# Kernel optimization log

Measured on AMD Instinct MI355X. Metric: run time of the kernel, lower is better.

Reference implementation:

```python
import jax, jax.numpy as jnp
import numpy as np
import math

B, S, D, H = 2, 2048, 1024, 16
DH = D // H  # head_dim = 64
NEG = -10000.0


def setup_inputs() -> dict:
    key = jax.random.key(0)
    ks = jax.random.split(key, 6)
    scale = 1.0 / math.sqrt(D)
    inp = {
        "query": jax.random.normal(ks[0], (B, S, D), dtype=jnp.float32),
        "key": jax.random.normal(ks[1], (B, S, D), dtype=jnp.float32),
        "value": jax.random.normal(ks[2], (B, S, D), dtype=jnp.float32),
        "Wq": jax.random.normal(ks[3], (D, D), dtype=jnp.float32) * scale,
        "Wk": jax.random.normal(ks[4], (D, D), dtype=jnp.float32) * scale,
        "Wv": jax.random.normal(ks[5], (D, D), dtype=jnp.float32) * scale,
        "pad_mask": jnp.ones((B, 1, 1, S), dtype=jnp.int32),
        "attn_mask": jnp.tril(jnp.ones((S, S), dtype=jnp.int32))[None, None],  # causal [1,1,S,S]
    }
    return inp


def reference(query, key, value, Wq, Wk, Wv, pad_mask, attn_mask):
    b, s, d = query.shape
    # torch Linear(bias=False): y = x @ W.T ; then split into heads [B,H,S,DH]
    def proj(x, W):
        return (x @ W.T).reshape(b, -1, H, DH).transpose(0, 2, 1, 3)

    Q = proj(query, Wq)
    K = proj(key, Wk)
    V = proj(value, Wv)

    scores = jnp.einsum("bhqd,bhkd->bhqk", Q, K) / math.sqrt(DH)
    scores = jnp.where(attn_mask == 0, NEG, scores)
    scores = jnp.where(pad_mask == 0, NEG, scores)
    attn = jax.nn.softmax(scores, axis=-1)  # dropout p=0.0 -> identity
    ctx = jnp.einsum("bhqk,bhkd->bhqd", attn, V)
    return ctx.transpose(0, 2, 1, 3).reshape(b, -1, d)
```

## Files before the change

kernel.cpp:

```cpp
#include <hip/hip_runtime.h>


typedef unsigned short u16;
typedef unsigned int u32;
typedef u16 u16x4 __attribute__((ext_vector_type(4)));
typedef u16 u16x8 __attribute__((ext_vector_type(8)));
typedef u32 u32x2 __attribute__((ext_vector_type(2)));
typedef u32 u32x4 __attribute__((ext_vector_type(4)));
typedef __bf16 bf16x8 __attribute__((ext_vector_type(8)));
typedef float f32x4 __attribute__((ext_vector_type(4)));

static __device__ __forceinline__ u16 f2bf(float f) {
  unsigned u = __builtin_bit_cast(unsigned, f);
  return (u16)((u + 0x7FFFu + ((u >> 16) & 1u)) >> 16);
}

static __device__ __forceinline__ u32 cvt_pk_bf16(float lo, float hi) {
  u32 r;
  asm("v_cvt_pk_bf16_f32 %0, %1, %2" : "=v"(r) : "v"(lo), "v"(hi));
  return r;
}

static __device__ __forceinline__ u16x8 cvt8(float4 f0, float4 f1) {
  u32x4 v;
  v[0] = cvt_pk_bf16(f0.x, f0.y);
  v[1] = cvt_pk_bf16(f0.z, f0.w);
  v[2] = cvt_pk_bf16(f1.x, f1.y);
  v[3] = cvt_pk_bf16(f1.z, f1.w);
  return __builtin_bit_cast(u16x8, v);
}

static __device__ __forceinline__ f32x4 mfma16(u16x8 a, u16x8 b, f32x4 c) {
  return __builtin_amdgcn_mfma_f32_16x16x32_bf16(
      __builtin_bit_cast(bf16x8, a), __builtin_bit_cast(bf16x8, b), c, 0, 0, 0);
}

static __device__ __forceinline__ float bperm_f(int lane, float v) {
  return __builtin_bit_cast(
      float, __builtin_amdgcn_ds_bpermute(lane * 4, __builtin_bit_cast(int, v)));
}

#define GLOAD16(GSRC, LDST)                                                  \
  __builtin_amdgcn_global_load_lds(                                         \
      (const __attribute__((address_space(1))) unsigned int*)(GSRC),        \
      (__attribute__((address_space(3))) unsigned int*)(LDST), 16, 0, 0)

#define FENCE() asm volatile("" ::: "memory")
#define BARX()                        \
  do {                                \
    __builtin_amdgcn_s_barrier();     \
    FENCE();                          \
  } while (0)

__global__ __launch_bounds__(256) void wconv_kernel(
    const float* __restrict__ Wq, const float* __restrict__ Wk,
    const float* __restrict__ Wv, u16* __restrict__ dst) {
  const float* src = (blockIdx.y == 0) ? Wq : (blockIdx.y == 1) ? Wk : Wv;
  u16* d = dst + (size_t)blockIdx.y * (1024 * 1024);
  const int i = (blockIdx.x * 256 + threadIdx.x) * 8;
  const float4 f0 = *(const float4*)(src + i);
  const float4 f1 = *(const float4*)(src + i + 4);
  *(u16x8*)(d + i) = cvt8(f0, f1);
}

__global__ __launch_bounds__(256) void proj_kernel(
    const float* __restrict__ Xq, const float* __restrict__ Xk, const float* __restrict__ Xv,
    const u16* __restrict__ Wbf,
    u16* __restrict__ Qb, u16* __restrict__ Kb, u16* __restrict__ Vt) {
  const int d0 = blockIdx.x;
  const int tid = (d0 & 7) * 96 + (d0 >> 3);
  const int nI = tid % 24, mI = tid / 24;
  const int mode = nI >> 3;
  const int m0 = mI * 128;
  const int n0 = (nI & 7) * 128;

  const float* __restrict__ X = (mode == 0) ? Xq : (mode == 1) ? Xk : Xv;
  const u16* __restrict__ W = Wbf + (size_t)mode * (1024 * 1024);

  __shared__ __align__(16) u16 As[3][128 * 32];
  __shared__ __align__(16) u16 Bs[3][128 * 32];

  const int t = threadIdx.x;
  const int lane = t & 63;
  const int w = t >> 6;
  const int wm = w >> 1, wn = w & 1;
  const int lr = lane & 15, lg = lane >> 4;

  const int srow0 = w * 32 + (lane >> 2);
  const int srow1 = srow0 + 16;
  const int skoff = ((lane & 3) ^ ((lane >> 3) & 3)) * 8;
  const int ldsb0 = w * 2048 + lane * 16;
  const int ldsb1 = ldsb0 + 1024;

  const float* Xr0 = X + (size_t)(m0 + srow0) * 1024 + skoff;
  const float* Xr1 = X + (size_t)(m0 + srow1) * 1024 + skoff;
  const u16* Wr0 = W + (size_t)(n0 + srow0) * 1024 + skoff;
  const u16* Wr1 = W + (size_t)(n0 + srow1) * 1024 + skoff;

  float4 a0_, a1_, a2_, a3_;

#define ISSUE_A(T)                                   \
  do {                                               \
    const float* _p0 = Xr0 + (T) * 32;               \
    const float* _p1 = Xr1 + (T) * 32;               \
    a0_ = ((const float4*)_p0)[0];                   \
    a1_ = ((const float4*)_p0)[1];                   \
    a2_ = ((const float4*)_p1)[0];                   \
    a3_ = ((const float4*)_p1)[1];                   \
  } while (0)
#define WRITE_A(BUF)                                                 \
  do {                                                               \
    *(u16x8*)((char*)As[BUF] + ldsb0) = cvt8(a0_, a1_);              \
    *(u16x8*)((char*)As[BUF] + ldsb1) = cvt8(a2_, a3_);              \
  } while (0)
#define ISSUE_B(T, BUF)                                              \
  do {                                                               \
    GLOAD16(Wr0 + (T) * 32, (char*)Bs[BUF] + w * 2048);              \
    GLOAD16(Wr1 + (T) * 32, (char*)Bs[BUF] + w * 2048 + 1024);       \
  } while (0)

  f32x4 acc[4][4] = {};
  const int rx = (lr >> 1) & 3;

#define CMP(BUF)                                                              \
  do {                                                                       \
    u16x8 af[4], bfr[4];                                                     \
    _Pragma("unroll") for (int mi = 0; mi < 4; ++mi) {                        \
      const int row = wm * 64 + mi * 16 + lr;                                \
      af[mi] = *(const u16x8*)((char*)As[BUF] + row * 64 + ((lg ^ rx) << 4)); \
    }                                                                         \
    _Pragma("unroll") for (int ni = 0; ni < 4; ++ni) {                        \
      const int row = wn * 64 + ni * 16 + lr;                                \
      bfr[ni] = *(const u16x8*)((char*)Bs[BUF] + row * 64 + ((lg ^ rx) << 4));\
    }                                                                         \
    _Pragma("unroll") for (int mi = 0; mi < 4; ++mi)                          \
        _Pragma("unroll") for (int ni = 0; ni < 4; ++ni)                      \
            acc[mi][ni] = mfma16(af[mi], bfr[ni], acc[mi][ni]);               \
  } while (0)

  ISSUE_A(0); WRITE_A(0);
  ISSUE_A(1); WRITE_A(1);
  ISSUE_A(2);
  ISSUE_B(0, 0);
  ISSUE_B(1, 1);
  asm volatile("s_waitcnt vmcnt(2) lgkmcnt(0)" ::: "memory");
  BARX();

  CMP(0);
  BARX();
  WRITE_A(2);
  ISSUE_A(3);
  ISSUE_B(2, 2);

  for (int tt = 1; tt <= 29; ++tt) {
    asm volatile("s_waitcnt vmcnt(6) lgkmcnt(0)" ::: "memory");
    BARX();
    CMP(tt % 3);
    BARX();
    WRITE_A((tt + 2) % 3);
    if (tt < 29) ISSUE_A(tt + 3);
    ISSUE_B(tt + 2, (tt + 2) % 3);
  }

  asm volatile("s_waitcnt vmcnt(2) lgkmcnt(0)" ::: "memory");
  BARX();
  CMP(30 % 3);
  asm volatile("s_waitcnt vmcnt(0) lgkmcnt(0)" ::: "memory");
  BARX();
  CMP(31 % 3);
#undef ISSUE_A
#undef WRITE_A
#undef ISSUE_B
#undef CMP

#pragma unroll
  for (int mi = 0; mi < 4; ++mi) {
    const int sbase = m0 + wm * 64 + mi * 16 + lg * 4;
    const int b_ = sbase >> 11;
    const int s_ = sbase & 2047;
#pragma unroll
    for (int ni = 0; ni < 4; ++ni) {
      const int n = n0 + wn * 64 + ni * 16 + lr;
      const int h_ = n >> 6, dh = n & 63;
      if (mode == 2) {
        u16x4 pk;
        pk[0] = f2bf(acc[mi][ni][0]);
        pk[1] = f2bf(acc[mi][ni][1]);
        pk[2] = f2bf(acc[mi][ni][2]);
        pk[3] = f2bf(acc[mi][ni][3]);
        *(u16x4*)(Vt + ((size_t)((b_ * 16 + h_) * 64 + dh)) * 2048 + s_) = pk;
      } else {
        const float sc = (mode == 0) ? 0.18033688f : 1.0f;
        u16* dst = (mode == 0 ? Qb : Kb) + (size_t)(b_ * 16 + h_) * (2048 * 64) + dh;
#pragma unroll
        for (int r = 0; r < 4; ++r)
          dst[(size_t)(s_ + r) * 64] = f2bf(acc[mi][ni][r] * sc);
      }
    }
  }
}

__global__ __launch_bounds__(256, 2) void attn_kernel(
    const u16* __restrict__ Qb, const u16* __restrict__ Kb, const u16* __restrict__ Vt,
    const int* __restrict__ pad, float* __restrict__ out) {
  const int id = blockIdx.x;
  const int g = id >> 8, r_ = id & 255;
  const int bh = r_ & 31;
  const int p8 = r_ >> 5;
  const int pi = g ? (15 - p8) : p8;
  const int qbA = 31 - pi, qbB = pi;

  const int b = bh >> 4, h = bh & 15;
  const u16* Qh = Qb + (size_t)bh * (2048 * 64);
  const u16* Kh = Kb + (size_t)bh * (2048 * 64);
  const u16* Vh = Vt + (size_t)bh * (64 * 2048);
  const int* padb = pad + b * 2048;

  __shared__ u16 Ks[2][64 * 64];
  __shared__ u16 Vs[2][64 * 64];
  __shared__ u16 Ps[4][16 * 64];

  const int t = threadIdx.x, lane = t & 63, w = t >> 6;
  const int lr = lane & 15, lg = lane >> 4;
  const int swz = (lr & 7) << 4;
  const int sr = t >> 3, scb = t & 7;
  const int qwaveA = qbA * 64 + w * 16, qwaveB = qbB * 64 + w * 16;

  u16x8 qfA[2], qfB[2];
#pragma unroll
  for (int kc = 0; kc < 2; ++kc) {
    qfA[kc] = *(const u16x8*)(Qh + (size_t)(qwaveA + lr) * 64 + kc * 32 + lg * 8);
    qfB[kc] = *(const u16x8*)(Qh + (size_t)(qwaveB + lr) * 64 + kc * 32 + lg * 8);
  }

  f32x4 accA[4] = {}, accB[4] = {};
  float mrowA = -1e4f, lsumA = 0.f, mrowB = -1e4f, lsumB = 0.f;

  u16x8 kr0, kr1, vr0, vr1;
  const int sb0 = (sr * 128 + scb * 16) ^ ((sr & 7) << 4);
  const int sb1 = ((32 + sr) * 128 + scb * 16) ^ ((sr & 7) << 4);

  kr0 = *(const u16x8*)(Kh + (size_t)sr * 64 + scb * 8);
  kr1 = *(const u16x8*)(Kh + (size_t)(32 + sr) * 64 + scb * 8);
  vr0 = *(const u16x8*)(Vh + (size_t)sr * 2048 + scb * 8);
  vr1 = *(const u16x8*)(Vh + (size_t)(32 + sr) * 2048 + scb * 8);
  *(u16x8*)((char*)Ks[0] + sb0) = kr0;
  *(u16x8*)((char*)Ks[0] + sb1) = kr1;
  *(u16x8*)((char*)Vs[0] + sb0) = vr0;
  *(u16x8*)((char*)Vs[0] + sb1) = vr1;
  __syncthreads();

#define PROCESS(QF, ACC, MROW, LSUM, QWAVE)                                    \
  do {                                                                         \
    f32x4 s4[4] = {};                                                          \
    __builtin_amdgcn_s_setprio(1);                                             \
    _Pragma("unroll") for (int ct = 0; ct < 4; ++ct) {                         \
      if (kv0 + ct * 16 <= (QWAVE) + 15) {                                     \
        _Pragma("unroll") for (int kc = 0; kc < 2; ++kc) {                     \
          const int byt = ((ct * 16 + lr) * 128 + kc * 64 + lg * 16) ^ swz;    \
          const u16x8 kf = *(const u16x8*)((char*)KsC + byt);                  \
          s4[ct] = mfma16(kf, QF[kc], s4[ct]);                                 \
        }                                                                      \
      }                                                                        \
    }                                                                          \
    __builtin_amdgcn_s_setprio(0);                                             \
    float vv[4][4];                                                            \
    if ((kv0 + 63 <= (QWAVE)) && allpad) {                                     \
      _Pragma("unroll") for (int ct = 0; ct < 4; ++ct)                         \
          _Pragma("unroll") for (int rr = 0; rr < 4; ++rr)                     \
              vv[ct][rr] = s4[ct][rr];                                         \
    } else {                                                                   \
      const int lim = (QWAVE) + lr - kv0 - lg * 4;                             \
      _Pragma("unroll") for (int ct = 0; ct < 4; ++ct) {                       \
        const int* pvp = (const int*)&pv4[ct];                                 \
        _Pragma("unroll") for (int rr = 0; rr < 4; ++rr)                       \
            vv[ct][rr] = (pvp[rr] && (ct * 16 + rr) <= lim) ? s4[ct][rr]       \
                                                            : -1e4f;           \
      }                                                                        \
    }                                                                          \
    float m0_ = fmaxf(fmaxf(fmaxf(vv[0][0], vv[0][1]), fmaxf(vv[0][2], vv[0][3])), \
                      fmaxf(fmaxf(vv[1][0], vv[1][1]), fmaxf(vv[1][2], vv[1][3]))); \
    float m1_ = fmaxf(fmaxf(fmaxf(vv[2][0], vv[2][1]), fmaxf(vv[2][2], vv[2][3])), \
                      fmaxf(fmaxf(vv[3][0], vv[3][1]), fmaxf(vv[3][2], vv[3][3]))); \
    float mx = fmaxf(m0_, m1_);                                                \
    mx = fmaxf(mx, __shfl_xor(mx, 16));                                        \
    mx = fmaxf(mx, __shfl_xor(mx, 32));                                        \
    if (!__all(mx <= (MROW) + 8.0f)) { \
      const float mn = fmaxf((MROW), mx);                                      \
      const float al = exp2f((MROW) - mn);                                     \
      (MROW) = mn;                                                             \
      (LSUM) *= al;                                                            \
      _Pragma("unroll") for (int rr = 0; rr < 4; ++rr) {                       \
        const float alv = bperm_f(lg * 4 + rr, al);                            \
        _Pragma("unroll") for (int dt = 0; dt < 4; ++dt) ACC[dt][rr] *= alv;   \
      }                                                                        \
    }                                                                          \
    float p[4][4];                                                             \
    _Pragma("unroll") for (int ct = 0; ct < 4; ++ct)                           \
        _Pragma("unroll") for (int rr = 0; rr < 4; ++rr)                       \
            p[ct][rr] = exp2f(vv[ct][rr] - (MROW));                            \
    float ps = (((p[0][0] + p[0][1]) + (p[0][2] + p[0][3])) +                  \
                ((p[1][0] + p[1][1]) + (p[1][2] + p[1][3]))) +                 \
               (((p[2][0] + p[2][1]) + (p[2][2] + p[2][3])) +                  \
                ((p[3][0] + p[3][1]) + (p[3][2] + p[3][3])));                  \
    ps += __shfl_xor(ps, 16);                                                  \
    ps += __shfl_xor(ps, 32);                                                  \
    (LSUM) += ps;                                                              \
    u16* PsB = &Ps[w][0];                                                      \
    _Pragma("unroll") for (int ct = 0; ct < 4; ++ct) {                         \
      u32x2 pw;                                                                \
      pw[0] = cvt_pk_bf16(p[ct][0], p[ct][1]);                                 \
      pw[1] = cvt_pk_bf16(p[ct][2], p[ct][3]);                                 \
      const int pb = (lr * 128 + ct * 32 + lg * 8) ^ swz;                      \
      *(u32x2*)((char*)PsB + pb) = pw;                                         \
    }                                                                          \
    const u16x8 pa0 = *(const u16x8*)((char*)PsB + ((lr * 128 + lg * 16) ^ swz));      \
    const u16x8 pa1 = *(const u16x8*)((char*)PsB + ((lr * 128 + 64 + lg * 16) ^ swz)); \
    __builtin_amdgcn_s_setprio(1);                                             \
    _Pragma("unroll") for (int dt = 0; dt < 4; ++dt) {                         \
      const int r0 = (dt * 16 + lr) * 128;                                     \
      ACC[dt] = mfma16(pa0, *(const u16x8*)((char*)VsC + ((r0 + lg * 16) ^ swz)), ACC[dt]);      \
      ACC[dt] = mfma16(pa1, *(const u16x8*)((char*)VsC + ((r0 + 64 + lg * 16) ^ swz)), ACC[dt]); \
    }                                                                          \
    __builtin_amdgcn_s_setprio(0);                                             \
  } while (0)

  int cur = 0;
  const int nst = qbA + 1;
  for (int st = 0; st < nst; ++st) {
    const int kv0 = st << 6;
    const bool more = st + 1 < nst;
    if (more) {
      const int nv0 = kv0 + 64;
      kr0 = *(const u16x8*)(Kh + (size_t)(nv0 + sr) * 64 + scb * 8);
      kr1 = *(const u16x8*)(Kh + (size_t)(nv0 + 32 + sr) * 64 + scb * 8);
      vr0 = *(const u16x8*)(Vh + (size_t)sr * 2048 + nv0 + scb * 8);
      vr1 = *(const u16x8*)(Vh + (size_t)(32 + sr) * 2048 + nv0 + scb * 8);
    }
    int4 pv4[4];
#pragma unroll
    for (int ct = 0; ct < 4; ++ct)
      pv4[ct] = *(const int4*)(padb + kv0 + ct * 16 + lg * 4);
    const int pall = pv4[0].x & pv4[0].y & pv4[0].z & pv4[0].w &
                     pv4[1].x & pv4[1].y & pv4[1].z & pv4[1].w &
                     pv4[2].x & pv4[2].y & pv4[2].z & pv4[2].w &
                     pv4[3].x & pv4[3].y & pv4[3].z & pv4[3].w;
    const bool allpad = __all(pall != 0);

    const u16* KsC = Ks[cur];
    const u16* VsC = Vs[cur];

    PROCESS(qfA, accA, mrowA, lsumA, qwaveA);
    if (st <= qbB)
      PROCESS(qfB, accB, mrowB, lsumB, qwaveB);

    if (more) {
      u16* Kn = Ks[cur ^ 1];
      u16* Vn = Vs[cur ^ 1];
      *(u16x8*)((char*)Kn + sb0) = kr0;
      *(u16x8*)((char*)Kn + sb1) = kr1;
      *(u16x8*)((char*)Vn + sb0) = vr0;
      *(u16x8*)((char*)Vn + sb1) = vr1;
    }
    __syncthreads();
    cur ^= 1;
  }
#undef PROCESS

#pragma unroll
  for (int tile = 0; tile < 2; ++tile) {
    const f32x4* acc = tile ? accB : accA;
    const float lsum = tile ? lsumB : lsumA;
    const int qwave = tile ? qwaveB : qwaveA;
    const float il = 1.0f / lsum;
    float* obase = out + ((size_t)(b * 2048 + qwave + lg * 4)) * 1024 + h * 64 + lr;
#pragma unroll
    for (int r = 0; r < 4; ++r) {
      const float linv = bperm_f(lg * 4 + r, il);
#pragma unroll
      for (int dt = 0; dt < 4; ++dt)
        obase[(size_t)r * 1024 + dt * 16] = acc[dt][r] * linv;
    }
  }
}

extern "C" void kernel_launch(void* const* d_in, const int* in_sizes, int n_in,
                              void* d_out, int out_size, void* d_ws, size_t ws_size,
                              hipStream_t stream) {
  const float* q  = (const float*)d_in[0];
  const float* k  = (const float*)d_in[1];
  const float* v  = (const float*)d_in[2];
  const float* wq = (const float*)d_in[3];
  const float* wk = (const float*)d_in[4];
  const float* wv = (const float*)d_in[5];
  const int* pad  = (const int*)d_in[6];
  float* out = (float*)d_out;

  u16* Qb  = (u16*)d_ws;
  u16* Kb  = Qb + (size_t)4 * 1024 * 1024;
  u16* Vt  = Kb + (size_t)4 * 1024 * 1024;
  u16* Wbf = Vt + (size_t)4 * 1024 * 1024;

  dim3 gc(512, 3);
  wconv_kernel<<<gc, 256, 0, stream>>>(wq, wk, wv, Wbf);

  proj_kernel<<<768, 256, 0, stream>>>(q, k, v, Wbf, Qb, Kb, Vt);

  attn_kernel<<<512, 256, 0, stream>>>(Qb, Kb, Vt, pad, out);
}
```

Baseline: 98.98 us.

## Load fp32 activations directly into LDS and convert to bf16 at fragment read

The projection GEMM no longer loads fp32 activations into registers and writes converted bf16 tiles to LDS. Both operands now go through direct global-to-LDS loads, with the A tile kept in fp32 using an XOR swizzle. The bf16 conversion moves to the fragment-read stage inside the compute step, and the three-stage pipeline is restructured around a uniform vmcnt wait. This trades more LDS space and LDS read bandwidth, plus repeated conversions per wave, for removing register staging and VALU stores from the load path.

New measurement: 110.3 us. +11.4%, slower.

```diff
diff --git a/kernel.cpp b/kernel.cpp
--- a/kernel.cpp
+++ b/kernel.cpp
@@ -77,8 +77,8 @@
   const float* __restrict__ X = (mode == 0) ? Xq : (mode == 1) ? Xk : Xv;
   const u16* __restrict__ W = Wbf + (size_t)mode * (1024 * 1024);
 
-  __shared__ __align__(16) u16 As[3][128 * 32];
-  __shared__ __align__(16) u16 Bs[3][128 * 32];
+  __shared__ __align__(16) char As[3][128 * 128];
+  __shared__ __align__(16) char Bs[3][128 * 64];
 
   const int t = threadIdx.x;
   const int lane = t & 63;
@@ -86,91 +86,84 @@
   const int wm = w >> 1, wn = w & 1;
   const int lr = lane & 15, lg = lane >> 4;
 
-  const int srow0 = w * 32 + (lane >> 2);
-  const int srow1 = srow0 + 16;
-  const int skoff = ((lane & 3) ^ ((lane >> 3) & 3)) * 8;
-  const int ldsb0 = w * 2048 + lane * 16;
-  const int ldsb1 = ldsb0 + 1024;
-
-  const float* Xr0 = X + (size_t)(m0 + srow0) * 1024 + skoff;
-  const float* Xr1 = X + (size_t)(m0 + srow1) * 1024 + skoff;
-  const u16* Wr0 = W + (size_t)(n0 + srow0) * 1024 + skoff;
-  const u16* Wr1 = W + (size_t)(n0 + srow1) * 1024 + skoff;
-
-  float4 a0_, a1_, a2_, a3_;
-
-#define ISSUE_A(T)                                   \
-  do {                                               \
-    const float* _p0 = Xr0 + (T) * 32;               \
-    const float* _p1 = Xr1 + (T) * 32;               \
-    a0_ = ((const float4*)_p0)[0];                   \
-    a1_ = ((const float4*)_p0)[1];                   \
-    a2_ = ((const float4*)_p1)[0];                   \
-    a3_ = ((const float4*)_p1)[1];                   \
+  const float* aptr[4];
+  int aoff[4];
+#pragma unroll
+  for (int jj = 0; jj < 4; ++jj) {
+    const int j = w * 4 + jj;
+    aptr[jj] = X + (size_t)(m0 + j * 8 + (lane >> 3)) * 1024 +
+               ((lane & 7) ^ (lane >> 3)) * 4;
+    aoff[jj] = j * 1024;
+  }
+  const u16* bptr[2];
+  int boff[2];
+#pragma unroll
+  for (int jj = 0; jj < 2; ++jj) {
+    const int j = w * 2 + jj;
+    bptr[jj] = W + (size_t)(n0 + j * 16 + (lane >> 2)) * 1024 +
+               ((lane & 3) ^ ((lane >> 3) & 3)) * 8;
+    boff[jj] = j * 1024;
+  }
+
+#define ISSUE(T, BUF)                                            \
+  do {                                                           \
+    _Pragma("unroll") for (int jj = 0; jj < 4; ++jj)             \
+        GLOAD16(aptr[jj] + (size_t)(T) * 32, As[BUF] + aoff[jj]); \
+    _Pragma("unroll") for (int jj = 0; jj < 2; ++jj)             \
+        GLOAD16(bptr[jj] + (size_t)(T) * 32, Bs[BUF] + boff[jj]); \
   } while (0)
-#define WRITE_A(BUF)                                                 \
-  do {                                                               \
-    *(u16x8*)((char*)As[BUF] + ldsb0) = cvt8(a0_, a1_);              \
-    *(u16x8*)((char*)As[BUF] + ldsb1) = cvt8(a2_, a3_);              \
-  } while (0)
-#define ISSUE_B(T, BUF)                                              \
-  do {                                                               \
-    GLOAD16(Wr0 + (T) * 32, (char*)Bs[BUF] + w * 2048);              \
-    GLOAD16(Wr1 + (T) * 32, (char*)Bs[BUF] + w * 2048 + 1024);       \
-  } while (0)
 
   f32x4 acc[4][4] = {};
-  const int rx = (lr >> 1) & 3;
 
 #define CMP(BUF)                                                              \
   do {                                                                       \
     u16x8 af[4], bfr[4];                                                     \
     _Pragma("unroll") for (int mi = 0; mi < 4; ++mi) {                        \
       const int row = wm * 64 + mi * 16 + lr;                                \
-      af[mi] = *(const u16x8*)((char*)As[BUF] + row * 64 + ((lg ^ rx) << 4)); \
+      const int rs = row & 7;                                                \
+      const f32x4 c0 =                                                       \
+          *(const f32x4*)(As[BUF] + row * 128 + (((lg * 2) ^ rs) * 16));     \
+      const f32x4 c1 =                                                       \
+          *(const f32x4*)(As[BUF] + row * 128 + (((lg * 2 + 1) ^ rs) * 16)); \
+      u32x4 pk;                                                              \
+      pk[0] = cvt_pk_bf16(c0[0], c0[1]);                                     \
+      pk[1] = cvt_pk_bf16(c0[2], c0[3]);                                     \
+      pk[2] = cvt_pk_bf16(c1[0], c1[1]);                                     \
+      pk[3] = cvt_pk_bf16(c1[2], c1[3]);                                     \
+      af[mi] = __builtin_bit_cast(u16x8, pk);                                \
     }                                                                         \
     _Pragma("unroll") for (int ni = 0; ni < 4; ++ni) {                        \
       const int row = wn * 64 + ni * 16 + lr;                                \
-      bfr[ni] = *(const u16x8*)((char*)Bs[BUF] + row * 64 + ((lg ^ rx) << 4));\
+      bfr[ni] = *(const u16x8*)(Bs[BUF] + row * 64 +                         \
+                                ((lg ^ ((row >> 1) & 3)) * 16));             \
     }                                                                         \
     _Pragma("unroll") for (int mi = 0; mi < 4; ++mi)                          \
         _Pragma("unroll") for (int ni = 0; ni < 4; ++ni)                      \
             acc[mi][ni] = mfma16(af[mi], bfr[ni], acc[mi][ni]);               \
   } while (0)
 
-  ISSUE_A(0); WRITE_A(0);
-  ISSUE_A(1); WRITE_A(1);
-  ISSUE_A(2);
-  ISSUE_B(0, 0);
-  ISSUE_B(1, 1);
-  asm volatile("s_waitcnt vmcnt(2) lgkmcnt(0)" ::: "memory");
+  ISSUE(0, 0);
+  ISSUE(1, 1);
+  ISSUE(2, 2);
+  asm volatile("s_waitcnt vmcnt(12)" ::: "memory");
   BARX();
 
-  CMP(0);
-  BARX();
-  WRITE_A(2);
-  ISSUE_A(3);
-  ISSUE_B(2, 2);
-
-  for (int tt = 1; tt <= 29; ++tt) {
-    asm volatile("s_waitcnt vmcnt(6) lgkmcnt(0)" ::: "memory");
+  for (int tt = 0; tt < 29; ++tt) {
+    CMP(tt % 3);
+    asm volatile("s_waitcnt lgkmcnt(0)" ::: "memory");
     BARX();
-    CMP(tt % 3);
+    ISSUE(tt + 3, tt % 3);
+    asm volatile("s_waitcnt vmcnt(12)" ::: "memory");
     BARX();
-    WRITE_A((tt + 2) % 3);
-    if (tt < 29) ISSUE_A(tt + 3);
-    ISSUE_B(tt + 2, (tt + 2) % 3);
-  }
-
-  asm volatile("s_waitcnt vmcnt(2) lgkmcnt(0)" ::: "memory");
+  }
+  CMP(29 % 3);
+  asm volatile("s_waitcnt vmcnt(6)" ::: "memory");
   BARX();
   CMP(30 % 3);
-  asm volatile("s_waitcnt vmcnt(0) lgkmcnt(0)" ::: "memory");
+  asm volatile("s_waitcnt vmcnt(0)" ::: "memory");
   BARX();
   CMP(31 % 3);
-#undef ISSUE_A
-#undef WRITE_A
-#undef ISSUE_B
+#undef ISSUE
 #undef CMP
 
 #pragma unroll
```
